# Optimization experiments

Hardware: AMD Instinct MI355X
Metric: run time of the kernel (lower is better)

The kernel has to match this reference:

```python
import jax, jax.numpy as jnp
import numpy as np

IN_C, HID, OUT_C = 768, 568, 1024
EPS = 1e-5

def _ln(x, g, b):
    mu = jnp.mean(x, axis=-1, keepdims=True)
    var = jnp.var(x, axis=-1, keepdims=True)
    return (x - mu) / jnp.sqrt(var + EPS) * g + b

def setup_inputs() -> dict:
    key = jax.random.key(0)
    ks = jax.random.split(key, 20)
    def lin(k, fan_in, fan_out):
        bound = 1.0 / np.sqrt(fan_in)
        kw, kb = jax.random.split(k)
        w = jax.random.uniform(kw, (fan_in, fan_out), jnp.float32, -bound, bound)
        b = jax.random.uniform(kb, (fan_out,), jnp.float32, -bound, bound)
        return w, b
    x = jax.random.normal(ks[0], (4, 2048, IN_C), jnp.float32)
    w_mlp, b_mlp = lin(ks[1], IN_C, HID)
    wq, bq = lin(ks[2], HID, OUT_C)
    wk, bk = lin(ks[3], HID, OUT_C)
    wv, bv = lin(ks[4], HID, OUT_C)
    wm, bm = lin(ks[5], HID, OUT_C)
    wf1, bf1 = lin(ks[6], OUT_C, OUT_C)
    wf2, bf2 = lin(ks[7], OUT_C, OUT_C)
    g1 = jnp.ones((OUT_C,), jnp.float32); be1 = jnp.zeros((OUT_C,), jnp.float32)
    g2 = jnp.ones((OUT_C,), jnp.float32); be2 = jnp.zeros((OUT_C,), jnp.float32)
    return dict(x=x, w_mlp=w_mlp, b_mlp=b_mlp, wq=wq, bq=bq, wk=wk, bk=bk,
                wv=wv, bv=bv, wm=wm, bm=bm, g1=g1, be1=be1,
                wf1=wf1, bf1=bf1, wf2=wf2, bf2=bf2, g2=g2, be2=be2)

def reference(x, w_mlp, b_mlp, wq, bq, wk, bk, wv, bv, wm, bm,
              g1, be1, wf1, bf1, wf2, bf2, g2, be2):
    # Joint.mlp: Linear + ReLU  -> h: [B, S, HID]
    h = jax.nn.relu(jnp.einsum('bsi,ih->bsh', x, w_mlp) + b_mlp)
    # Block: single-head attention (dropout=eval -> identity)
    q = jnp.einsum('bsh,hd->bsd', h, wq) + bq
    k = jnp.einsum('bsh,hd->bsd', h, wk) + bk
    v = jnp.einsum('bsh,hd->bsd', h, wv) + bv
    scale = 1.0 / jnp.sqrt(jnp.float32(OUT_C))
    attn = jax.nn.softmax(jnp.einsum('bqd,bkd->bqk', q, k) * scale, axis=-1)
    attn_out = jnp.einsum('bqk,bkd->bqd', attn, v)
    x_mod = jnp.einsum('bsh,hd->bsd', h, wm) + bm
    x1 = _ln(x_mod + attn_out, g1, be1)
    ffn = jnp.einsum('bsd,de->bse', jax.nn.relu(jnp.einsum('bsd,de->bse', x1, wf1) + bf1), wf2) + bf2
    x2 = _ln(x1 + ffn, g2, be2)
    # trailing ReLU in Joint.attn Sequential
    return jax.nn.relu(x2)
```

## Files before the change

### kernel.cpp

```cpp
#include <hip/hip_runtime.h>

#define DI __device__ __forceinline__

typedef unsigned short u16;
typedef __attribute__((__ext_vector_type__(8))) __bf16 bf16x8;
typedef __attribute__((__ext_vector_type__(4))) float f32x4;
typedef __attribute__((__ext_vector_type__(4))) unsigned short u16x4;
typedef __attribute__((__ext_vector_type__(8))) unsigned short u16x8;

DI float bf2f(u16 u) { union { unsigned int i; float f; } x; x.i = ((unsigned int)u) << 16; return x.f; }
DI u16 f2bf(float f) {
  union { float f; unsigned int i; } x; x.f = f;
  unsigned int r = x.i + 0x7fffu + ((x.i >> 16) & 1u);
  return (u16)(r >> 16);
}

DI void gload_lds16(const void* g, void* lds) {
  __builtin_amdgcn_global_load_lds((const __attribute__((address_space(1))) unsigned int*)g,
                                   (__attribute__((address_space(3))) unsigned int*)lds, 16, 0, 0);
}

template<bool RELU, bool OUT_BF16, bool HAS_BIAS>
__global__ __launch_bounds__(512, 4)
void gemm128(const u16* __restrict__ A, long long sAb, int lda,
             const u16* __restrict__ Bt, long long sBb, int ldb,
             const float* __restrict__ bias,
             void* __restrict__ C, long long sCb, int ldc,
             int K, float scale)
{
  __shared__ __align__(16) u16 lds[24576];

  const int tid = threadIdx.x;
  const int w = tid >> 6, l = tid & 63;
  const int wm = w >> 2, wn = w & 3;

  const int gx = gridDim.x;
  const int nwg = gx * gridDim.y;
  const int f = blockIdx.x + gx * blockIdx.y;
  const int fs = (f & 7) * (nwg >> 3) + (f >> 3);
  const int bx = fs % gx, by = fs / gx;

  const long long bm = (long long)by * 128;
  const long long bn = (long long)bx * 256;
  const u16* Ab = A + (long long)blockIdx.z * sAb;
  const u16* Btb = Bt + (long long)blockIdx.z * sBb;

  const int ia = w * 64 + l;
  const int ra = ia >> 2;
  const int ga = (ia & 3) ^ ((ra >> 1) & 3);
  const u16* pA  = Ab  + (bm + ra) * (long long)lda + ga * 8;
  const u16* pB0 = Btb + (bn + ra) * (long long)ldb + ga * 8;
  const u16* pB1 = Btb + (bn + 128 + ra) * (long long)ldb + ga * 8;
  u16* dA  = lds + w * 512;
  u16* dB0 = lds + 4096 + w * 512;
  u16* dB1 = lds + 8192 + w * 512;

  const int swz = ((l >> 4) ^ (((l & 15) >> 1) & 3)) << 3;
  const int aOff = (wm * 64 + (l & 15)) * 32 + swz;
  const int bOff = 4096 + (wn * 64 + (l & 15)) * 32 + swz;

  f32x4 acc[4][4] = {};
  const int NKT = K >> 5;

  gload_lds16(pA, dA);        gload_lds16(pB0, dB0);        gload_lds16(pB1, dB1);
  gload_lds16(pA + 32, dA + 12288); gload_lds16(pB0 + 32, dB0 + 12288); gload_lds16(pB1 + 32, dB1 + 12288);

  for (int kt = 0; kt < NKT; ++kt) {
    if (kt + 1 < NKT) asm volatile("s_waitcnt vmcnt(3)" ::: "memory");
    else              asm volatile("s_waitcnt vmcnt(0)" ::: "memory");
    __builtin_amdgcn_s_barrier();
    __builtin_amdgcn_sched_barrier(0);

    const u16* bufc = lds + (kt & 1) * 12288;
    bf16x8 aF[4], bF[4];
    #pragma unroll
    for (int mf = 0; mf < 4; ++mf) aF[mf] = *(const bf16x8*)(bufc + aOff + mf * 512);
    #pragma unroll
    for (int nf = 0; nf < 4; ++nf) bF[nf] = *(const bf16x8*)(bufc + bOff + nf * 512);
    asm volatile("s_waitcnt lgkmcnt(0)" ::: "memory");
    __builtin_amdgcn_s_barrier();
    __builtin_amdgcn_sched_barrier(0);

    if (kt + 2 < NKT) {
      u16* d = lds + (kt & 1) * 12288 + w * 512;
      const long long ko = (long long)(kt + 2) * 32;
      gload_lds16(pA + ko, d);
      gload_lds16(pB0 + ko, d + 4096);
      gload_lds16(pB1 + ko, d + 8192);
    }
    __builtin_amdgcn_s_setprio(1);
    #pragma unroll
    for (int mf = 0; mf < 4; ++mf)
      #pragma unroll
      for (int nf = 0; nf < 4; ++nf)
        acc[mf][nf] = __builtin_amdgcn_mfma_f32_16x16x32_bf16(aF[mf], bF[nf], acc[mf][nf], 0, 0, 0);
    __builtin_amdgcn_s_setprio(0);
  }

  float bias4[4];
  if (HAS_BIAS) {
    #pragma unroll
    for (int nf = 0; nf < 4; ++nf) bias4[nf] = bias[bn + wn * 64 + (l & 15) + nf * 16];
  }
  float* fl = (float*)lds + w * 1024;
  const long long cbase = (long long)blockIdx.z * sCb;
  const int colq = (l & 15) * 4;
  #pragma unroll
  for (int mf = 0; mf < 4; ++mf) {
    #pragma unroll
    for (int nf = 0; nf < 4; ++nf) {
      #pragma unroll
      for (int r = 0; r < 4; ++r) {
        float v = acc[mf][nf][r] * scale;
        if (HAS_BIAS) v += bias4[nf];
        if (RELU) v = fmaxf(v, 0.f);
        fl[((l >> 4) * 4 + r) * 64 + (l & 15) + nf * 16] = v;
      }
    }
    asm volatile("s_waitcnt lgkmcnt(0)" ::: "memory");
    #pragma unroll
    for (int p = 0; p < 4; ++p) {
      f32x4 v = *(const f32x4*)(fl + p * 256 + l * 4);
      const long long row = bm + wm * 64 + mf * 16 + p * 4 + (l >> 4);
      const long long cidx = cbase + row * ldc + bn + wn * 64 + colq;
      if (OUT_BF16) {
        u16x4 o; o.x = f2bf(v.x); o.y = f2bf(v.y); o.z = f2bf(v.z); o.w = f2bf(v.w);
        *(u16x4*)((u16*)C + cidx) = o;
      } else {
        *(f32x4*)((float*)C + cidx) = v;
      }
    }
    asm volatile("s_waitcnt lgkmcnt(0)" ::: "memory");
  }
}

__global__ void transpose_cast_pad(const float* __restrict__ in, int inR, int inC,
                                   u16* __restrict__ out, int outR, int outC)
{
  __shared__ float tile[32][33];
  const int c0 = blockIdx.x * 32;
  const int r0 = blockIdx.y * 32;
  const int tx = threadIdx.x, ty = threadIdx.y;
  for (int i = ty; i < 32; i += 8) {
    int r = r0 + i, c = c0 + tx;
    tile[i][tx] = (r < inR && c < inC) ? in[(long long)r * inC + c] : 0.f;
  }
  __syncthreads();
  for (int i = ty; i < 32; i += 8) {
    int orow = c0 + i, ocol = r0 + tx;
    if (orow < outR && ocol < outC)
      out[(long long)orow * outC + ocol] = f2bf(tile[tx][i]);
  }
}

__global__ void transpose_bf16_k(const u16* __restrict__ in, long long sIb, int ldi,
                                 u16* __restrict__ out, long long sOb, int ldo)
{
  __shared__ u16 tile[32][33];
  const u16* inp = in + (long long)blockIdx.z * sIb;
  u16* outp = out + (long long)blockIdx.z * sOb;
  const int r0 = blockIdx.y * 32, c0 = blockIdx.x * 32;
  const int tx = threadIdx.x, ty = threadIdx.y;
  for (int i = ty; i < 32; i += 8)
    tile[i][tx] = inp[(long long)(r0 + i) * ldi + c0 + tx];
  __syncthreads();
  for (int i = ty; i < 32; i += 8)
    outp[(long long)(c0 + i) * ldo + r0 + tx] = tile[tx][i];
}

__global__ void cast_f32_bf16_k(const float* __restrict__ in, u16* __restrict__ out, int n4)
{
  int i = blockIdx.x * blockDim.x + threadIdx.x;
  if (i >= n4) return;
  float4 v = ((const float4*)in)[i];
  u16x4 o; o.x = f2bf(v.x); o.y = f2bf(v.y); o.z = f2bf(v.z); o.w = f2bf(v.w);
  ((u16x4*)out)[i] = o;
}

__global__ void prep_bias_k(const float* __restrict__ bmlp, const float* __restrict__ bq,
                            const float* __restrict__ bk, const float* __restrict__ bv,
                            const float* __restrict__ bm,
                            float* __restrict__ outMlp, float* __restrict__ outQkvm)
{
  int i = blockIdx.x * 256 + threadIdx.x;
  if (i < 768) outMlp[i] = (i < 568) ? bmlp[i] : 0.f;
  if (i < 4096) {
    const float* s = (i < 1024) ? bq : (i < 2048) ? bk : (i < 3072) ? bv : bm;
    outQkvm[i] = s[i & 1023];
  }
}

__global__ __launch_bounds__(256)
void softmax_rows_k(u16* __restrict__ sc)
{
  __shared__ float red[8];
  const long long base = (long long)blockIdx.x * 2048;
  const int t = threadIdx.x, wave = t >> 6, lane = t & 63;
  u16x8 v8 = *((const u16x8*)(sc + base + t * 8));
  float v[8];
  #pragma unroll
  for (int j = 0; j < 8; ++j) v[j] = bf2f(v8[j]);
  float m = v[0];
  #pragma unroll
  for (int j = 1; j < 8; ++j) m = fmaxf(m, v[j]);
  #pragma unroll
  for (int off = 32; off > 0; off >>= 1) m = fmaxf(m, __shfl_xor(m, off, 64));
  if (lane == 0) red[wave] = m;
  __syncthreads();
  m = fmaxf(fmaxf(red[0], red[1]), fmaxf(red[2], red[3]));
  float s = 0.f;
  #pragma unroll
  for (int j = 0; j < 8; ++j) { v[j] = __expf(v[j] - m); s += v[j]; }
  #pragma unroll
  for (int off = 32; off > 0; off >>= 1) s += __shfl_xor(s, off, 64);
  if (lane == 0) red[4 + wave] = s;
  __syncthreads();
  s = red[4] + red[5] + red[6] + red[7];
  float inv = 1.f / s;
  u16x8 o;
  #pragma unroll
  for (int j = 0; j < 8; ++j) o[j] = f2bf(v[j] * inv);
  *((u16x8*)(sc + base + t * 8)) = o;
}

__global__ __launch_bounds__(256)
void add_ln_k(const u16* __restrict__ a, int lda, const float* __restrict__ b,
              const float* __restrict__ gamma, const float* __restrict__ beta,
              u16* __restrict__ out)
{
  __shared__ float red[8];
  const long long row = blockIdx.x;
  const int t = threadIdx.x, wave = t >> 6, lane = t & 63;
  u16x4 av = *((const u16x4*)(a + row * lda + t * 4));
  float4 bv = ((const float4*)(b + row * 1024))[t];
  float z[4] = { bf2f(av.x) + bv.x, bf2f(av.y) + bv.y, bf2f(av.z) + bv.z, bf2f(av.w) + bv.w };
  float s = z[0] + z[1] + z[2] + z[3];
  float ss = z[0]*z[0] + z[1]*z[1] + z[2]*z[2] + z[3]*z[3];
  #pragma unroll
  for (int off = 32; off > 0; off >>= 1) { s += __shfl_xor(s, off, 64); ss += __shfl_xor(ss, off, 64); }
  if (lane == 0) { red[wave] = s; red[4 + wave] = ss; }
  __syncthreads();
  s = red[0] + red[1] + red[2] + red[3];
  ss = red[4] + red[5] + red[6] + red[7];
  float mu = s * (1.f / 1024.f);
  float var = ss * (1.f / 1024.f) - mu * mu;
  float rstd = rsqrtf(var + 1e-5f);
  float4 g = ((const float4*)gamma)[t];
  float4 be = ((const float4*)beta)[t];
  u16x4 o;
  o.x = f2bf((z[0] - mu) * rstd * g.x + be.x);
  o.y = f2bf((z[1] - mu) * rstd * g.y + be.y);
  o.z = f2bf((z[2] - mu) * rstd * g.z + be.z);
  o.w = f2bf((z[3] - mu) * rstd * g.w + be.w);
  *((u16x4*)(out + row * 1024 + t * 4)) = o;
}

__global__ __launch_bounds__(256)
void add_ln_relu_k(const u16* __restrict__ a, const float* __restrict__ b,
                   const float* __restrict__ gamma, const float* __restrict__ beta,
                   float* __restrict__ out)
{
  __shared__ float red[8];
  const long long row = blockIdx.x;
  const int t = threadIdx.x, wave = t >> 6, lane = t & 63;
  u16x4 av = *((const u16x4*)(a + row * 1024 + t * 4));
  float4 bv = ((const float4*)(b + row * 1024))[t];
  float z[4] = { bf2f(av.x) + bv.x, bf2f(av.y) + bv.y, bf2f(av.z) + bv.z, bf2f(av.w) + bv.w };
  float s = z[0] + z[1] + z[2] + z[3];
  float ss = z[0]*z[0] + z[1]*z[1] + z[2]*z[2] + z[3]*z[3];
  #pragma unroll
  for (int off = 32; off > 0; off >>= 1) { s += __shfl_xor(s, off, 64); ss += __shfl_xor(ss, off, 64); }
  if (lane == 0) { red[wave] = s; red[4 + wave] = ss; }
  __syncthreads();
  s = red[0] + red[1] + red[2] + red[3];
  ss = red[4] + red[5] + red[6] + red[7];
  float mu = s * (1.f / 1024.f);
  float var = ss * (1.f / 1024.f) - mu * mu;
  float rstd = rsqrtf(var + 1e-5f);
  float4 g = ((const float4*)gamma)[t];
  float4 be = ((const float4*)beta)[t];
  float4 o;
  o.x = fmaxf((z[0] - mu) * rstd * g.x + be.x, 0.f);
  o.y = fmaxf((z[1] - mu) * rstd * g.y + be.y, 0.f);
  o.z = fmaxf((z[2] - mu) * rstd * g.z + be.z, 0.f);
  o.w = fmaxf((z[3] - mu) * rstd * g.w + be.w, 0.f);
  ((float4*)(out + row * 1024))[t] = o;
}

extern "C" void kernel_launch(void* const* d_in, const int* in_sizes, int n_in,
                              void* d_out, int out_size, void* d_ws, size_t ws_size,
                              hipStream_t stream)
{
  const float* x    = (const float*)d_in[0];
  const float* wmlp = (const float*)d_in[1];
  const float* bmlp = (const float*)d_in[2];
  const float* wq   = (const float*)d_in[3];  const float* bq  = (const float*)d_in[4];
  const float* wk   = (const float*)d_in[5];  const float* bk  = (const float*)d_in[6];
  const float* wv   = (const float*)d_in[7];  const float* bv  = (const float*)d_in[8];
  const float* wm   = (const float*)d_in[9];  const float* bm  = (const float*)d_in[10];
  const float* g1   = (const float*)d_in[11]; const float* be1 = (const float*)d_in[12];
  const float* wf1  = (const float*)d_in[13]; const float* bf1 = (const float*)d_in[14];
  const float* wf2  = (const float*)d_in[15]; const float* bf2 = (const float*)d_in[16];
  const float* g2   = (const float*)d_in[17]; const float* be2 = (const float*)d_in[18];

  char* ws = (char*)d_ws;
  size_t off = 0;
  auto alloc = [&](size_t bytes) { char* p = ws + off; off += (bytes + 255) & ~(size_t)255; return p; };
  u16*  W_MLP_T  = (u16*)alloc((size_t)768 * 768 * 2);
  u16*  W_QKVM_T = (u16*)alloc((size_t)4096 * 768 * 2);
  u16*  W_F1_T   = (u16*)alloc((size_t)1024 * 1024 * 2);
  u16*  W_F2_T   = (u16*)alloc((size_t)1024 * 1024 * 2);
  float* B_MLP   = (float*)alloc(768 * 4);
  float* B_QKVM  = (float*)alloc(4096 * 4);
  u16*  XBF      = (u16*)alloc((size_t)8192 * 768 * 2);
  u16*  H        = (u16*)alloc((size_t)8192 * 768 * 2);
  u16*  QKVM     = (u16*)alloc((size_t)8192 * 4096 * 2);
  u16*  VT       = (u16*)alloc((size_t)4 * 1024 * 2048 * 2);
  u16*  SC       = (u16*)alloc((size_t)4 * 2048 * 2048 * 2);
  float* AO      = (float*)alloc((size_t)8192 * 1024 * 4);
  u16*  X1       = (u16*)alloc((size_t)8192 * 1024 * 2);
  u16*  T  = QKVM;
  float* F = (float*)((char*)QKVM + (size_t)8192 * 2048 * 2);

  dim3 tb(32, 8);

  cast_f32_bf16_k<<<(8192 * 768 / 4 + 255) / 256, 256, 0, stream>>>(x, XBF, 8192 * 768 / 4);
  transpose_cast_pad<<<dim3(24, 24), tb, 0, stream>>>(wmlp, 768, 568, W_MLP_T, 768, 768);
  transpose_cast_pad<<<dim3(32, 24), tb, 0, stream>>>(wq, 568, 1024, W_QKVM_T + (size_t)0 * 1024 * 768, 1024, 768);
  transpose_cast_pad<<<dim3(32, 24), tb, 0, stream>>>(wk, 568, 1024, W_QKVM_T + (size_t)1 * 1024 * 768, 1024, 768);
  transpose_cast_pad<<<dim3(32, 24), tb, 0, stream>>>(wv, 568, 1024, W_QKVM_T + (size_t)2 * 1024 * 768, 1024, 768);
  transpose_cast_pad<<<dim3(32, 24), tb, 0, stream>>>(wm, 568, 1024, W_QKVM_T + (size_t)3 * 1024 * 768, 1024, 768);
  transpose_cast_pad<<<dim3(32, 32), tb, 0, stream>>>(wf1, 1024, 1024, W_F1_T, 1024, 1024);
  transpose_cast_pad<<<dim3(32, 32), tb, 0, stream>>>(wf2, 1024, 1024, W_F2_T, 1024, 1024);
  prep_bias_k<<<16, 256, 0, stream>>>(bmlp, bq, bk, bv, bm, B_MLP, B_QKVM);

  gemm128<true, true, true><<<dim3(3, 64, 1), 512, 0, stream>>>(
      XBF, 0, 768, W_MLP_T, 0, 768, B_MLP, H, 0, 768, 768, 1.0f);
  gemm128<false, true, true><<<dim3(16, 64, 1), 512, 0, stream>>>(
      H, 0, 768, W_QKVM_T, 0, 768, B_QKVM, QKVM, 0, 4096, 768, 1.0f);
  transpose_bf16_k<<<dim3(32, 64, 4), tb, 0, stream>>>(
      QKVM + 2048, (long long)2048 * 4096, 4096, VT, (long long)1024 * 2048, 2048);
  gemm128<false, true, false><<<dim3(8, 16, 4), 512, 0, stream>>>(
      QKVM, (long long)2048 * 4096, 4096, QKVM + 1024, (long long)2048 * 4096, 4096,
      nullptr, SC, (long long)2048 * 2048, 2048, 1024, 0.03125f);
  softmax_rows_k<<<8192, 256, 0, stream>>>(SC);
  gemm128<false, false, false><<<dim3(4, 16, 4), 512, 0, stream>>>(
      SC, (long long)2048 * 2048, 2048, VT, (long long)1024 * 2048, 2048,
      nullptr, AO, (long long)2048 * 1024, 1024, 2048, 1.0f);
  add_ln_k<<<8192, 256, 0, stream>>>(QKVM + 3072, 4096, AO, g1, be1, X1);
  gemm128<true, true, true><<<dim3(4, 64, 1), 512, 0, stream>>>(
      X1, 0, 1024, W_F1_T, 0, 1024, bf1, T, 0, 1024, 1024, 1.0f);
  gemm128<false, false, true><<<dim3(4, 64, 1), 512, 0, stream>>>(
      T, 0, 1024, W_F2_T, 0, 1024, bf2, F, 0, 1024, 1024, 1.0f);
  add_ln_relu_k<<<8192, 256, 0, stream>>>(X1, F, g2, be2, (float*)d_out);
}
```

Before: 297.1 us.

## Add 256x256-tile GEMM for QKVM projection and attention scores, trim K padding

```diff
diff --git a/kernel.cpp b/kernel.cpp
--- a/kernel.cpp
+++ b/kernel.cpp
@@ -18,6 +18,157 @@
 DI void gload_lds16(const void* g, void* lds) {
   __builtin_amdgcn_global_load_lds((const __attribute__((address_space(1))) unsigned int*)g,
                                    (__attribute__((address_space(3))) unsigned int*)lds, 16, 0, 0);
+}
+
+template<bool RELU, bool OUT_BF16, bool HAS_BIAS>
+__global__ __launch_bounds__(512, 2)
+void gemm256v2(const u16* __restrict__ A, long long sAb, int lda,
+               const u16* __restrict__ Bt, long long sBb, int ldb,
+               const float* __restrict__ bias,
+               void* __restrict__ C, long long sCb, int ldc,
+               int K, float scale)
+{
+  extern __shared__ __align__(16) u16 lds[];
+
+  const int tid = threadIdx.x;
+  const int w = tid >> 6, l = tid & 63;
+  const int wm = w >> 2, wn = w & 3;
+
+  const int gx = gridDim.x;
+  const int nwg = gx * gridDim.y;
+  const int f = blockIdx.x + gx * blockIdx.y;
+  const int fs = (f & 7) * (nwg >> 3) + (f >> 3);
+  const int bx = fs % gx, by = fs / gx;
+
+  const long long bm = (long long)by * 256;
+  const long long bn = (long long)bx * 256;
+  const u16* Ab = A + (long long)blockIdx.z * sAb;
+  const u16* Btb = Bt + (long long)blockIdx.z * sBb;
+
+  const int trow = tid >> 3;
+  const int tg = (tid & 7) ^ (trow & 7);
+  const u16* sA = Ab + (bm + trow) * (long long)lda + tg * 8;
+  const u16* sB = Btb + (bn + trow) * (long long)ldb + tg * 8;
+  const long long la64 = (long long)64 * lda, lb64 = (long long)64 * ldb;
+
+  const int swz0 = (((l >> 4) ^ (l & 7))) * 8;
+  const int aB = (wm * 128 + (l & 15)) * 64;
+  const int bB = 16384 + (wn * 64 + (l & 15)) * 64;
+
+  f32x4 acc[8][4] = {};
+  const int NKT = K >> 6;
+
+  {
+    u16* sp = lds;
+    gload_lds16(sA, sp + w * 512);
+    gload_lds16(sA + 2 * la64, sp + 8192 + w * 512);
+    gload_lds16(sB, sp + 16384 + w * 512);
+    gload_lds16(sB + lb64, sp + 20480 + w * 512);
+    gload_lds16(sB + 2 * lb64, sp + 24576 + w * 512);
+    gload_lds16(sB + 3 * lb64, sp + 28672 + w * 512);
+    gload_lds16(sA + la64, sp + 4096 + w * 512);
+    gload_lds16(sA + 3 * la64, sp + 12288 + w * 512);
+  }
+
+  for (int kt = 0; kt < NKT; ++kt) {
+    const u16* bp = lds + (kt & 1) * 32768;
+    u16* sp = lds + ((kt & 1) ^ 1) * 32768;
+    const bool st = (kt + 1) < NKT;
+    const long long ko = (long long)(kt + 1) * 64;
+
+    asm volatile("s_waitcnt vmcnt(2)" ::: "memory");
+    __builtin_amdgcn_s_barrier();
+
+    if (st) {
+      gload_lds16(sA + ko, sp + w * 512);
+      gload_lds16(sA + 2 * la64 + ko, sp + 8192 + w * 512);
+      gload_lds16(sB + ko, sp + 16384 + w * 512);
+      gload_lds16(sB + lb64 + ko, sp + 20480 + w * 512);
+      gload_lds16(sB + 2 * lb64 + ko, sp + 24576 + w * 512);
+      gload_lds16(sB + 3 * lb64 + ko, sp + 28672 + w * 512);
+    }
+
+    bf16x8 bF[4][2], aF[4][2];
+    #pragma unroll
+    for (int nf = 0; nf < 4; ++nf) {
+      bF[nf][0] = *(const bf16x8*)(bp + bB + nf * 1024 + swz0);
+      bF[nf][1] = *(const bf16x8*)(bp + bB + nf * 1024 + (swz0 ^ 32));
+    }
+    #pragma unroll
+    for (int mf = 0; mf < 4; ++mf) {
+      aF[mf][0] = *(const bf16x8*)(bp + aB + mf * 1024 + swz0);
+      aF[mf][1] = *(const bf16x8*)(bp + aB + mf * 1024 + (swz0 ^ 32));
+    }
+    if (st) {
+      gload_lds16(sA + la64 + ko, sp + 4096 + w * 512);
+      gload_lds16(sA + 3 * la64 + ko, sp + 12288 + w * 512);
+    }
+    __builtin_amdgcn_s_setprio(1);
+    #pragma unroll
+    for (int mf = 0; mf < 4; ++mf)
+      #pragma unroll
+      for (int nf = 0; nf < 4; ++nf) {
+        acc[mf][nf] = __builtin_amdgcn_mfma_f32_16x16x32_bf16(aF[mf][0], bF[nf][0], acc[mf][nf], 0, 0, 0);
+        acc[mf][nf] = __builtin_amdgcn_mfma_f32_16x16x32_bf16(aF[mf][1], bF[nf][1], acc[mf][nf], 0, 0, 0);
+      }
+    __builtin_amdgcn_s_setprio(0);
+
+    if (st) asm volatile("s_waitcnt vmcnt(8)" ::: "memory");
+    else    asm volatile("s_waitcnt vmcnt(0)" ::: "memory");
+    __builtin_amdgcn_s_barrier();
+
+    #pragma unroll
+    for (int mf = 0; mf < 4; ++mf) {
+      aF[mf][0] = *(const bf16x8*)(bp + aB + (mf + 4) * 1024 + swz0);
+      aF[mf][1] = *(const bf16x8*)(bp + aB + (mf + 4) * 1024 + (swz0 ^ 32));
+    }
+    __builtin_amdgcn_s_setprio(1);
+    #pragma unroll
+    for (int mf = 0; mf < 4; ++mf)
+      #pragma unroll
+      for (int nf = 0; nf < 4; ++nf) {
+        acc[mf + 4][nf] = __builtin_amdgcn_mfma_f32_16x16x32_bf16(aF[mf][0], bF[nf][0], acc[mf + 4][nf], 0, 0, 0);
+        acc[mf + 4][nf] = __builtin_amdgcn_mfma_f32_16x16x32_bf16(aF[mf][1], bF[nf][1], acc[mf + 4][nf], 0, 0, 0);
+      }
+    __builtin_amdgcn_s_setprio(0);
+  }
+
+  __syncthreads();
+  float bias4[4];
+  if (HAS_BIAS) {
+    #pragma unroll
+    for (int nf = 0; nf < 4; ++nf) bias4[nf] = bias[bn + wn * 64 + (l & 15) + nf * 16];
+  }
+  float* fl = (float*)lds + w * 1024;
+  const long long cbase = (long long)blockIdx.z * sCb;
+  const int colq = (l & 15) * 4;
+  #pragma unroll
+  for (int mf = 0; mf < 8; ++mf) {
+    #pragma unroll
+    for (int nf = 0; nf < 4; ++nf) {
+      #pragma unroll
+      for (int r = 0; r < 4; ++r) {
+        float v = acc[mf][nf][r] * scale;
+        if (HAS_BIAS) v += bias4[nf];
+        if (RELU) v = fmaxf(v, 0.f);
+        fl[((l >> 4) * 4 + r) * 64 + (l & 15) + nf * 16] = v;
+      }
+    }
+    asm volatile("s_waitcnt lgkmcnt(0)" ::: "memory");
+    #pragma unroll
+    for (int p = 0; p < 4; ++p) {
+      f32x4 v = *(const f32x4*)(fl + p * 256 + l * 4);
+      const long long row = bm + wm * 128 + mf * 16 + p * 4 + (l >> 4);
+      const long long cidx = cbase + row * ldc + bn + wn * 64 + colq;
+      if (OUT_BF16) {
+        u16x4 o; o.x = f2bf(v.x); o.y = f2bf(v.y); o.z = f2bf(v.z); o.w = f2bf(v.w);
+        *(u16x4*)((u16*)C + cidx) = o;
+      } else {
+        *(f32x4*)((float*)C + cidx) = v;
+      }
+    }
+    asm volatile("s_waitcnt lgkmcnt(0)" ::: "memory");
+  }
 }
 
 template<bool RELU, bool OUT_BF16, bool HAS_BIAS>
@@ -307,7 +458,7 @@
   size_t off = 0;
   auto alloc = [&](size_t bytes) { char* p = ws + off; off += (bytes + 255) & ~(size_t)255; return p; };
   u16*  W_MLP_T  = (u16*)alloc((size_t)768 * 768 * 2);
-  u16*  W_QKVM_T = (u16*)alloc((size_t)4096 * 768 * 2);
+  u16*  W_QKVM_T = (u16*)alloc((size_t)4096 * 640 * 2);
   u16*  W_F1_T   = (u16*)alloc((size_t)1024 * 1024 * 2);
   u16*  W_F2_T   = (u16*)alloc((size_t)1024 * 1024 * 2);
   float* B_MLP   = (float*)alloc(768 * 4);
@@ -322,25 +473,28 @@
   u16*  T  = QKVM;
   float* F = (float*)((char*)QKVM + (size_t)8192 * 2048 * 2);
 
+  hipFuncSetAttribute((const void*)gemm256v2<false, true, true >, hipFuncAttributeMaxDynamicSharedMemorySize, 131072);
+  hipFuncSetAttribute((const void*)gemm256v2<false, true, false>, hipFuncAttributeMaxDynamicSharedMemorySize, 131072);
+
   dim3 tb(32, 8);
 
   cast_f32_bf16_k<<<(8192 * 768 / 4 + 255) / 256, 256, 0, stream>>>(x, XBF, 8192 * 768 / 4);
   transpose_cast_pad<<<dim3(24, 24), tb, 0, stream>>>(wmlp, 768, 568, W_MLP_T, 768, 768);
-  transpose_cast_pad<<<dim3(32, 24), tb, 0, stream>>>(wq, 568, 1024, W_QKVM_T + (size_t)0 * 1024 * 768, 1024, 768);
-  transpose_cast_pad<<<dim3(32, 24), tb, 0, stream>>>(wk, 568, 1024, W_QKVM_T + (size_t)1 * 1024 * 768, 1024, 768);
-  transpose_cast_pad<<<dim3(32, 24), tb, 0, stream>>>(wv, 568, 1024, W_QKVM_T + (size_t)2 * 1024 * 768, 1024, 768);
-  transpose_cast_pad<<<dim3(32, 24), tb, 0, stream>>>(wm, 568, 1024, W_QKVM_T + (size_t)3 * 1024 * 768, 1024, 768);
+  transpose_cast_pad<<<dim3(32, 20), tb, 0, stream>>>(wq, 568, 1024, W_QKVM_T + (size_t)0 * 1024 * 640, 1024, 640);
+  transpose_cast_pad<<<dim3(32, 20), tb, 0, stream>>>(wk, 568, 1024, W_QKVM_T + (size_t)1 * 1024 * 640, 1024, 640);
+  transpose_cast_pad<<<dim3(32, 20), tb, 0, stream>>>(wv, 568, 1024, W_QKVM_T + (size_t)2 * 1024 * 640, 1024, 640);
+  transpose_cast_pad<<<dim3(32, 20), tb, 0, stream>>>(wm, 568, 1024, W_QKVM_T + (size_t)3 * 1024 * 640, 1024, 640);
   transpose_cast_pad<<<dim3(32, 32), tb, 0, stream>>>(wf1, 1024, 1024, W_F1_T, 1024, 1024);
   transpose_cast_pad<<<dim3(32, 32), tb, 0, stream>>>(wf2, 1024, 1024, W_F2_T, 1024, 1024);
   prep_bias_k<<<16, 256, 0, stream>>>(bmlp, bq, bk, bv, bm, B_MLP, B_QKVM);
 
   gemm128<true, true, true><<<dim3(3, 64, 1), 512, 0, stream>>>(
       XBF, 0, 768, W_MLP_T, 0, 768, B_MLP, H, 0, 768, 768, 1.0f);
-  gemm128<false, true, true><<<dim3(16, 64, 1), 512, 0, stream>>>(
-      H, 0, 768, W_QKVM_T, 0, 768, B_QKVM, QKVM, 0, 4096, 768, 1.0f);
+  gemm256v2<false, true, true><<<dim3(16, 32, 1), 512, 131072, stream>>>(
+      H, 0, 768, W_QKVM_T, 0, 640, B_QKVM, QKVM, 0, 4096, 640, 1.0f);
   transpose_bf16_k<<<dim3(32, 64, 4), tb, 0, stream>>>(
       QKVM + 2048, (long long)2048 * 4096, 4096, VT, (long long)1024 * 2048, 2048);
-  gemm128<false, true, false><<<dim3(8, 16, 4), 512, 0, stream>>>(
+  gemm256v2<false, true, false><<<dim3(8, 8, 4), 512, 131072, stream>>>(
       QKVM, (long long)2048 * 4096, 4096, QKVM + 1024, (long long)2048 * 4096, 4096,
       nullptr, SC, (long long)2048 * 2048, 2048, 1024, 0.03125f);
   softmax_rows_k<<<8192, 256, 0, stream>>>(SC);
```

New measurement: 281.2 us. 5.4% less time.
